# Optimization experiments

Hardware: AMD Instinct MI355X
Metric: run time of the kernel (lower is better)

Reference implementation:

```python
import jax, jax.numpy as jnp
import numpy as np

B, T, H, V, NT, NH, DFF = 2, 512, 768, 51865, 3, 4, 2048
EPS = 1e-5


def setup_inputs() -> dict:
    key = jax.random.key(0)
    ks = jax.random.split(key, 24)
    s = 0.02
    d = {
        "encoder_hidden": jax.random.normal(ks[0], (B, T, H), jnp.float32),
        "teacher_tokens": jax.random.randint(ks[1], (B, T, NT), 0, V, jnp.int32),
        "start_token": jax.random.normal(ks[2], (1, H), jnp.float32),
        "emb": jax.random.normal(ks[3], (V, H), jnp.float32) * s,
        # self-attention (torch MultiheadAttention packed qkv in_proj)
        "sa_in_w": jax.random.normal(ks[4], (3 * H, H), jnp.float32) * s,
        "sa_in_b": jnp.zeros((3 * H,), jnp.float32),
        "sa_out_w": jax.random.normal(ks[5], (H, H), jnp.float32) * s,
        "sa_out_b": jnp.zeros((H,), jnp.float32),
        # cross-attention
        "ca_in_w": jax.random.normal(ks[6], (3 * H, H), jnp.float32) * s,
        "ca_in_b": jnp.zeros((3 * H,), jnp.float32),
        "ca_out_w": jax.random.normal(ks[7], (H, H), jnp.float32) * s,
        "ca_out_b": jnp.zeros((H,), jnp.float32),
        # FFN
        "lin1_w": jax.random.normal(ks[8], (DFF, H), jnp.float32) * s,
        "lin1_b": jnp.zeros((DFF,), jnp.float32),
        "lin2_w": jax.random.normal(ks[9], (H, DFF), jnp.float32) * s,
        "lin2_b": jnp.zeros((H,), jnp.float32),
        # layer norms (post-norm TransformerDecoderLayer)
        "ln1_g": jnp.ones((H,), jnp.float32), "ln1_b": jnp.zeros((H,), jnp.float32),
        "ln2_g": jnp.ones((H,), jnp.float32), "ln2_b": jnp.zeros((H,), jnp.float32),
        "ln3_g": jnp.ones((H,), jnp.float32), "ln3_b": jnp.zeros((H,), jnp.float32),
        # output vocab projection (bias=False)
        "proj_w": jax.random.normal(ks[10], (V, H), jnp.float32) * s,
    }
    return d


def _ln(x, g, b):
    m = jnp.mean(x, -1, keepdims=True)
    v = jnp.mean(jnp.square(x - m), -1, keepdims=True)
    return (x - m) * jax.lax.rsqrt(v + EPS) * g + b


def _mha(xq, xkv, in_w, in_b, out_w, out_b, mask=None):
    # xq: (N, Lq, H), xkv: (N, Lk, H). torch packed in_proj: [Wq; Wk; Wv].
    h = xq.shape[-1]
    wq, wk, wv = jnp.split(in_w, 3, axis=0)
    bq, bk, bv = jnp.split(in_b, 3, axis=0)
    hd = h // NH
    q = (xq @ wq.T + bq).reshape(*xq.shape[:-1], NH, hd)
    k = (xkv @ wk.T + bk).reshape(*xkv.shape[:-1], NH, hd)
    v = (xkv @ wv.T + bv).reshape(*xkv.shape[:-1], NH, hd)
    scores = jnp.einsum("nqhd,nkhd->nhqk", q, k) / jnp.sqrt(jnp.float32(hd)).astype(q.dtype)
    if mask is not None:
        scores = scores + mask  # (Lq,Lk) additive causal mask
    a = jax.nn.softmax(scores, axis=-1)
    o = jnp.einsum("nhqk,nkhd->nqhd", a, v).reshape(*xq.shape[:-1], h)
    return o @ out_w.T + out_b


def _forward(encoder_hidden, teacher_tokens, start_token, emb,
             sa_in_w, sa_in_b, sa_out_w, sa_out_b,
             ca_in_w, ca_in_b, ca_out_w, ca_out_b,
             lin1_w, lin1_b, lin2_w, lin2_b,
             ln1_g, ln1_b, ln2_g, ln2_b, ln3_g, ln3_b, proj_w):
    b, t, h = encoder_hidden.shape
    nt = teacher_tokens.shape[-1]
    n = b * t
    # With teacher forcing + causal mask, step-i logits == position-i output of a
    # single decoder pass over [start, emb(teacher[..., :nt-1])] with memory of length 1.
    tok_emb = jnp.take(emb, teacher_tokens[:, :, : nt - 1], axis=0)  # (B,T,NT-1,H)
    start = jnp.broadcast_to(start_token.reshape(1, 1, 1, h), (b, t, 1, h))
    tgt = jnp.concatenate([start, tok_emb], axis=2).reshape(n, nt, h)  # (N,NT,H)
    mem = encoder_hidden.reshape(n, 1, h)  # (N,1,H)
    causal = jnp.where(jnp.triu(jnp.ones((nt, nt), bool), 1), -jnp.inf, 0.0).astype(tgt.dtype)
    # post-norm TransformerDecoderLayer (dropout=identity at eval)
    x = tgt
    x = _ln(x + _mha(x, x, sa_in_w, sa_in_b, sa_out_w, sa_out_b, causal), ln1_g, ln1_b)
    x = _ln(x + _mha(x, mem, ca_in_w, ca_in_b, ca_out_w, ca_out_b), ln2_g, ln2_b)
    ff = jax.nn.relu(x @ lin1_w.T + lin1_b) @ lin2_w.T + lin2_b
    x = _ln(x + ff, ln3_g, ln3_b)
    logits = x @ proj_w.T  # (N,NT,V)
    return logits.reshape(b, t, nt, -1)


def reference(encoder_hidden, teacher_tokens, start_token, emb,
              sa_in_w, sa_in_b, sa_out_w, sa_out_b,
              ca_in_w, ca_in_b, ca_out_w, ca_out_b,
              lin1_w, lin1_b, lin2_w, lin2_b,
              ln1_g, ln1_b, ln2_g, ln2_b, ln3_g, ln3_b, proj_w):
    return _forward(encoder_hidden, teacher_tokens, start_token, emb,
                    sa_in_w, sa_in_b, sa_out_w, sa_out_b,
                    ca_in_w, ca_in_b, ca_out_w, ca_out_b,
                    lin1_w, lin1_b, lin2_w, lin2_b,
                    ln1_g, ln1_b, ln2_g, ln2_b, ln3_g, ln3_b, proj_w)
```

## Files before the change

kernel.cpp:

```cpp
#include <hip/hip_runtime.h>

typedef __bf16 bf16;
typedef __bf16 bf16x4 __attribute__((ext_vector_type(4)));
typedef __bf16 bf16x8 __attribute__((ext_vector_type(8)));
typedef float f32x4 __attribute__((ext_vector_type(4)));

#define BM 128
#define BN 128
#define BK 32

__device__ __forceinline__ void async16(const void* g, void* l) {
    __builtin_amdgcn_global_load_lds(
        (__attribute__((address_space(1))) void*)g,
        (__attribute__((address_space(3))) void*)l,
        16, 0, 0);
}

__device__ __forceinline__ void stageA256(const bf16* A, int K, int brow, int r0,
                                          int k0, bf16* ldsA, int t, int wid) {
    int lr = t >> 3;
    int c  = (t & 7) ^ (lr & 7);
    const bf16* g = A + (size_t)(brow + r0 + lr) * K + k0 + c * 8;
    async16(g, ldsA + r0 * 64 + wid * 512);
}

__device__ __forceinline__ void stageB256(const bf16* W, int K, int bcol, int j,
                                          int k0, bf16* ldsB, int t, int wid) {
    int lr  = t >> 3;
    int R   = j * 64 + lr;
    int col = ((R >> 5) & 3) * 64 + (R >> 7) * 32 + (R & 31);
    int c   = (t & 7) ^ (lr & 7);
    const bf16* g = W + (size_t)(bcol + col) * K + k0 + c * 8;
    async16(g, ldsB + j * 4096 + wid * 512);
}

template<int VM, int QM, int QN>
__device__ __forceinline__ void mfma_phase256(const bf16* pa, const bf16* pb,
    int wm, int wn, int lane, f32x4 acc[8][4])
{
    const int l15 = lane & 15, l7 = lane & 7, lhi = lane >> 4;
    bf16x8 a[4][2], b[2][2];
    #pragma unroll
    for (int fi = 0; fi < 4; fi++)
        #pragma unroll
        for (int ks = 0; ks < 2; ks++)
            a[fi][ks] = *(const bf16x8*)(pa + (wm*128 + QM*64 + fi*16 + l15) * 64
                                            + ((ks*4 + lhi) ^ l7) * 8);
    #pragma unroll
    for (int fj = 0; fj < 2; fj++)
        #pragma unroll
        for (int ks = 0; ks < 2; ks++)
            b[fj][ks] = *(const bf16x8*)(pb + (QN*128 + wn*32 + fj*16 + l15) * 64
                                            + ((ks*4 + lhi) ^ l7) * 8);
    if (VM == 4)      asm volatile("s_waitcnt vmcnt(4)" ::: "memory");
    else if (VM == 2) asm volatile("s_waitcnt vmcnt(2)" ::: "memory");
    else              asm volatile("s_waitcnt vmcnt(0)" ::: "memory");
    __builtin_amdgcn_s_barrier();
    __builtin_amdgcn_s_setprio(1);
    #pragma unroll
    for (int fi = 0; fi < 4; fi++)
        #pragma unroll
        for (int fj = 0; fj < 2; fj++) {
            f32x4 c0 = acc[QM*4 + fi][QN*2 + fj];
            c0 = __builtin_amdgcn_mfma_f32_16x16x32_bf16(a[fi][0], b[fj][0], c0, 0,0,0);
            c0 = __builtin_amdgcn_mfma_f32_16x16x32_bf16(a[fi][1], b[fj][1], c0, 0,0,0);
            acc[QM*4 + fi][QN*2 + fj] = c0;
        }
    __builtin_amdgcn_s_setprio(0);
}

__global__ __launch_bounds__(512, 2) void gemm256(
    const bf16* __restrict__ A, const bf16* __restrict__ W,
    float* __restrict__ C, int K, int ldo, int Nstore, int nTilesM)
{
    __shared__ bf16 lds[2][2][16384];

    int nwg = gridDim.x;
    int orig = blockIdx.x;
    int q = nwg >> 3, r = nwg & 7, xcd = orig & 7, local = orig >> 3;
    int wgid = (xcd < r ? xcd * (q + 1) : r * (q + 1) + (xcd - r) * q) + local;
    const int brow = (wgid % nTilesM) * 256;
    const int bcol = (wgid / nTilesM) * 256;

    const int t = threadIdx.x;
    const int wid = t >> 6, lane = t & 63;
    const int wm = wid >> 2, wn = wid & 3;

    f32x4 acc[8][4] = {};
    const int nkt = K >> 6;

    {
        bf16* lA = &lds[0][0][0];
        bf16* lB = &lds[0][1][0];
        stageA256(A, K, brow,   0, 0, lA, t, wid);
        stageA256(A, K, brow, 128, 0, lA, t, wid);
        stageB256(W, K, bcol, 0, 0, lB, t, wid);
        stageB256(W, K, bcol, 1, 0, lB, t, wid);
        stageA256(A, K, brow,  64, 0, lA, t, wid);
        stageA256(A, K, brow, 192, 0, lA, t, wid);
        stageB256(W, K, bcol, 2, 0, lB, t, wid);
        stageB256(W, K, bcol, 3, 0, lB, t, wid);
        asm volatile("s_waitcnt vmcnt(4)" ::: "memory");
        __builtin_amdgcn_s_barrier();
    }

    for (int tt = 0; tt < nkt - 1; ++tt) {
        const int cur = tt & 1, nxt = cur ^ 1;
        const bf16* cA = &lds[cur][0][0];
        const bf16* cB = &lds[cur][1][0];
        bf16* nA = &lds[nxt][0][0];
        bf16* nB = &lds[nxt][1][0];
        const int k1 = (tt + 1) << 6;
        stageA256(A, K, brow,   0, k1, nA, t, wid);
        stageA256(A, K, brow, 128, k1, nA, t, wid);
        mfma_phase256<4, 0, 0>(cA, cB, wm, wn, lane, acc);
        stageB256(W, K, bcol, 0, k1, nB, t, wid);
        stageB256(W, K, bcol, 1, k1, nB, t, wid);
        mfma_phase256<4, 1, 0>(cA, cB, wm, wn, lane, acc);
        stageA256(A, K, brow,  64, k1, nA, t, wid);
        stageA256(A, K, brow, 192, k1, nA, t, wid);
        mfma_phase256<4, 0, 1>(cA, cB, wm, wn, lane, acc);
        stageB256(W, K, bcol, 2, k1, nB, t, wid);
        stageB256(W, K, bcol, 3, k1, nB, t, wid);
        mfma_phase256<4, 1, 1>(cA, cB, wm, wn, lane, acc);
    }
    {
        const int cur = (nkt - 1) & 1;
        const bf16* cA = &lds[cur][0][0];
        const bf16* cB = &lds[cur][1][0];
        mfma_phase256<2, 0, 0>(cA, cB, wm, wn, lane, acc);
        mfma_phase256<0, 1, 0>(cA, cB, wm, wn, lane, acc);
        mfma_phase256<0, 0, 1>(cA, cB, wm, wn, lane, acc);
        mfma_phase256<0, 1, 1>(cA, cB, wm, wn, lane, acc);
    }

    float* ldsf = (float*)&lds[0][0][0];
    const int l15 = lane & 15, lhi4 = (lane >> 4) * 4;
    #pragma unroll
    for (int h = 0; h < 2; h++) {
        __syncthreads();
        #pragma unroll
        for (int fi4 = 0; fi4 < 4; fi4++) {
            #pragma unroll
            for (int fj = 0; fj < 4; fj++) {
                f32x4 v = acc[h * 4 + fi4][fj];
                int row = wm * 64 + fi4 * 16 + lhi4;
                int col = wn * 64 + fj * 16 + l15;
                #pragma unroll
                for (int r2 = 0; r2 < 4; r2++)
                    ldsf[(row + r2) * 256 + col] = v[r2];
            }
        }
        __syncthreads();
        #pragma unroll
        for (int i = 0; i < 16; i++) {
            int c = i * 512 + t;
            int row = c >> 6, ch = c & 63;
            f32x4 v = *(const f32x4*)(ldsf + row * 256 + ch * 4);
            int grow = brow + (row >> 6) * 128 + h * 64 + (row & 63);
            int gcol = bcol + ch * 4;
            float* dst = C + (size_t)grow * ldo + gcol;
            if (gcol + 4 <= Nstore) {
                *(f32x4*)dst = v;
            } else {
                #pragma unroll
                for (int k2 = 0; k2 < 4; k2++)
                    if (gcol + k2 < Nstore) dst[k2] = v[k2];
            }
        }
    }
}

__global__ __launch_bounds__(256) void gemm_bt(
    const bf16* __restrict__ A, const bf16* __restrict__ W,
    const float* __restrict__ bias,
    float* __restrict__ outF, bf16* __restrict__ outB,
    int M, int K, int ldo, int Nstore, int relu)
{
    __shared__ bf16 As[BM * BK];
    __shared__ bf16 Ws[BN * BK];
    const int brow = blockIdx.y * BM;
    const int bcol = blockIdx.x * BN;
    const int t = threadIdx.x;
    const int wv = t >> 6;
    const int lane = t & 63;
    const int wrow = (wv >> 1) * 64;
    const int wcol = (wv & 1) * 64;

    f32x4 acc[4][4] = {};

    const int row0 = t >> 2;
    const int cg = (t & 3) * 8;
    const bf16* gA = A + (size_t)(brow + row0) * K + cg;
    const bf16* gW = W + (size_t)(bcol + row0) * K + cg;
    const size_t rstep = (size_t)64 * K;
    bf16* lA0 = As + wv * 512;
    bf16* lA1 = As + 2048 + wv * 512;
    bf16* lW0 = Ws + wv * 512;
    bf16* lW1 = Ws + 2048 + wv * 512;

    const int lrow = lane & 15;
    const int kg = (lane >> 4) * 8;

    for (int k0 = 0; k0 < K; k0 += BK) {
        if (k0) __syncthreads();
        async16(gA + k0, lA0);
        async16(gA + rstep + k0, lA1);
        async16(gW + k0, lW0);
        async16(gW + rstep + k0, lW1);
        __syncthreads();
        bf16x8 af[4], wf[4];
        #pragma unroll
        for (int i = 0; i < 4; i++)
            af[i] = *(const bf16x8*)(As + (wrow + i * 16 + lrow) * BK + kg);
        #pragma unroll
        for (int j = 0; j < 4; j++)
            wf[j] = *(const bf16x8*)(Ws + (wcol + j * 16 + lrow) * BK + kg);
        #pragma unroll
        for (int i = 0; i < 4; i++)
            #pragma unroll
            for (int j = 0; j < 4; j++)
                acc[i][j] = __builtin_amdgcn_mfma_f32_16x16x32_bf16(
                    af[i], wf[j], acc[i][j], 0, 0, 0);
    }

    const int lcol = lane & 15;
    const int rb = (lane >> 4) * 4;
    #pragma unroll
    for (int j = 0; j < 4; j++) {
        int n = bcol + wcol + j * 16 + lcol;
        if (n >= Nstore) continue;
        float bv = bias ? bias[n] : 0.f;
        #pragma unroll
        for (int i = 0; i < 4; i++) {
            #pragma unroll
            for (int r = 0; r < 4; r++) {
                int m = brow + wrow + i * 16 + rb + r;
                float v = acc[i][j][r] + bv;
                if (relu) v = fmaxf(v, 0.f);
                size_t off = (size_t)m * ldo + n;
                if (outF) outF[off] = v;
                if (outB) outB[off] = (bf16)v;
            }
        }
    }
}

__global__ __launch_bounds__(256) void cvt_bf16(
    const float* __restrict__ in, bf16* __restrict__ out,
    size_t nvalid, size_t ntotal)
{
    size_t i = ((size_t)blockIdx.x * 256 + threadIdx.x) * 4;
    if (i >= ntotal) return;
    bf16x4 r;
    if (i < nvalid) {
        f32x4 f = __builtin_nontemporal_load((const f32x4*)(in + i));
        r[0] = (bf16)f[0]; r[1] = (bf16)f[1]; r[2] = (bf16)f[2]; r[3] = (bf16)f[3];
    } else {
        r[0] = (bf16)0.f; r[1] = (bf16)0.f; r[2] = (bf16)0.f; r[3] = (bf16)0.f;
    }
    *(bf16x4*)(out + i) = r;
}

__global__ __launch_bounds__(256) void build_tgt(
    const float* __restrict__ start, const float* __restrict__ emb,
    const int* __restrict__ toks, float* __restrict__ outF, bf16* __restrict__ outB)
{
    int r = blockIdx.x;
    int n = r / 3, p = r % 3;
    const float* src = (p == 0) ? start : emb + (size_t)toks[n * 3 + (p - 1)] * 768;
    int t = threadIdx.x;
    #pragma unroll
    for (int j = 0; j < 3; j++) {
        int c = t + j * 256;
        float v = src[c];
        outF[(size_t)r * 768 + c] = v;
        outB[(size_t)r * 768 + c] = (bf16)v;
    }
}

__global__ __launch_bounds__(64) void attn3(
    const float* __restrict__ qkv, bf16* __restrict__ o)
{
    int blk = blockIdx.x;
    int n = blk >> 2, h = blk & 3;
    int lane = threadIdx.x;
    const float* base = qkv + (size_t)n * 3 * 2304 + h * 192;
    float q[3][3], k[3][3], v[3][3];
    #pragma unroll
    for (int p = 0; p < 3; p++)
        #pragma unroll
        for (int j = 0; j < 3; j++) {
            int d = lane + j * 64;
            q[p][j] = base[p * 2304 + d];
            k[p][j] = base[p * 2304 + 768 + d];
            v[p][j] = base[p * 2304 + 1536 + d];
        }
    float s[3][3];
    #pragma unroll
    for (int p = 0; p < 3; p++)
        #pragma unroll
        for (int pk = 0; pk < 3; pk++) {
            if (pk > p) continue;
            float ps = q[p][0] * k[pk][0] + q[p][1] * k[pk][1] + q[p][2] * k[pk][2];
            #pragma unroll
            for (int off = 32; off; off >>= 1) ps += __shfl_xor(ps, off);
            s[p][pk] = ps * 0.072168783648703220563f;
        }
    float a[3][3] = {};
    a[0][0] = 1.f;
    {
        float m = fmaxf(s[1][0], s[1][1]);
        float e0 = expf(s[1][0] - m), e1 = expf(s[1][1] - m);
        float inv = 1.f / (e0 + e1);
        a[1][0] = e0 * inv; a[1][1] = e1 * inv;
    }
    {
        float m = fmaxf(fmaxf(s[2][0], s[2][1]), s[2][2]);
        float e0 = expf(s[2][0] - m), e1 = expf(s[2][1] - m), e2 = expf(s[2][2] - m);
        float inv = 1.f / (e0 + e1 + e2);
        a[2][0] = e0 * inv; a[2][1] = e1 * inv; a[2][2] = e2 * inv;
    }
    bf16* ob = o + (size_t)n * 3 * 768 + h * 192;
    #pragma unroll
    for (int p = 0; p < 3; p++)
        #pragma unroll
        for (int j = 0; j < 3; j++) {
            float val = a[p][0] * v[0][j];
            if (p >= 1) val += a[p][1] * v[1][j];
            if (p >= 2) val += a[p][2] * v[2][j];
            ob[p * 768 + lane + j * 64] = (bf16)val;
        }
}

__global__ __launch_bounds__(256) void add_ln(
    const float* __restrict__ a, const float* __restrict__ b,
    const float* __restrict__ g, const float* __restrict__ be,
    float* __restrict__ outF, bf16* __restrict__ outB, int bcast)
{
    int r = blockIdx.x;
    int t = threadIdx.x;
    const float* ar = a + (size_t)r * 768;
    const float* br = b + (size_t)(bcast ? (r / 3) : r) * 768;
    float x[3];
    float s = 0.f, sq = 0.f;
    #pragma unroll
    for (int j = 0; j < 3; j++) {
        int c = t + j * 256;
        x[j] = ar[c] + br[c];
        s += x[j]; sq += x[j] * x[j];
    }
    #pragma unroll
    for (int off = 32; off; off >>= 1) {
        s += __shfl_xor(s, off);
        sq += __shfl_xor(sq, off);
    }
    __shared__ float ls[4], lq[4];
    int wv = t >> 6;
    if ((t & 63) == 0) { ls[wv] = s; lq[wv] = sq; }
    __syncthreads();
    s = ls[0] + ls[1] + ls[2] + ls[3];
    sq = lq[0] + lq[1] + lq[2] + lq[3];
    float mean = s * (1.f / 768.f);
    float var = sq * (1.f / 768.f) - mean * mean;
    float inv = rsqrtf(var + 1e-5f);
    #pragma unroll
    for (int j = 0; j < 3; j++) {
        int c = t + j * 256;
        float y = (x[j] - mean) * inv * g[c] + be[c];
        if (outF) outF[(size_t)r * 768 + c] = y;
        if (outB) outB[(size_t)r * 768 + c] = (bf16)y;
    }
}

static inline void run_gemm(const bf16* A, const bf16* W, const float* bias,
                            float* outF, bf16* outB, int M, int Npad, int K,
                            int ldo, int Nstore, int relu, hipStream_t s)
{
    dim3 grid(Npad / BN, M / BM);
    gemm_bt<<<grid, 256, 0, s>>>(A, W, bias, outF, outB, M, K, ldo, Nstore, relu);
}

static inline void run_cvt(const float* in, bf16* out, size_t nvalid,
                           size_t ntotal, hipStream_t s)
{
    int blocks = (int)((ntotal / 4 + 255) / 256);
    cvt_bf16<<<blocks, 256, 0, s>>>(in, out, nvalid, ntotal);
}

extern "C" void kernel_launch(void* const* d_in, const int* in_sizes, int n_in,
                              void* d_out, int out_size, void* d_ws, size_t ws_size,
                              hipStream_t stream)
{
    const float* enc      = (const float*)d_in[0];
    const int*   toks     = (const int*)d_in[1];
    const float* start    = (const float*)d_in[2];
    const float* emb      = (const float*)d_in[3];
    const float* sa_in_w  = (const float*)d_in[4];
    const float* sa_in_b  = (const float*)d_in[5];
    const float* sa_out_w = (const float*)d_in[6];
    const float* sa_out_b = (const float*)d_in[7];
    const float* ca_in_w  = (const float*)d_in[8];
    const float* ca_in_b  = (const float*)d_in[9];
    const float* ca_out_w = (const float*)d_in[10];
    const float* ca_out_b = (const float*)d_in[11];
    const float* lin1_w   = (const float*)d_in[12];
    const float* lin1_b   = (const float*)d_in[13];
    const float* lin2_w   = (const float*)d_in[14];
    const float* lin2_b   = (const float*)d_in[15];
    const float* ln1_g    = (const float*)d_in[16];
    const float* ln1_bb   = (const float*)d_in[17];
    const float* ln2_g    = (const float*)d_in[18];
    const float* ln2_bb   = (const float*)d_in[19];
    const float* ln3_g    = (const float*)d_in[20];
    const float* ln3_bb   = (const float*)d_in[21];
    const float* proj_w   = (const float*)d_in[22];
    float* out = (float*)d_out;

    const int NTOK = 3072;
    const int NM   = 1024;
    const int H    = 768;
    const int V    = 51865;
    const int VPAD = 51968;
    const int DFF  = 2048;

    char* p = (char*)d_ws;
    auto alloc = [&](size_t bytes) {
        void* r = (void*)p;
        p += (bytes + 255) & ~(size_t)255;
        return r;
    };
    float* tgt_f = (float*)alloc((size_t)NTOK * H * 4);
    float* x1_f  = (float*)alloc((size_t)NTOK * H * 4);
    float* x2_f  = (float*)alloc((size_t)NTOK * H * 4);
    float* big_f = (float*)alloc((size_t)NTOK * 2304 * 4);
    bf16*  actA  = (bf16*)alloc((size_t)NTOK * 2304 * 2);
    bf16*  actB  = (bf16*)alloc((size_t)NTOK * DFF * 2);
    bf16*  Wbf   = (bf16*)alloc((size_t)VPAD * H * 2);
    bf16*  mem_bf = actB;
    bf16*  v_bf   = actB + (size_t)NM * H;
    float* cao_f  = big_f + (size_t)NTOK * H;

    build_tgt<<<NTOK, 256, 0, stream>>>(start, emb, toks, tgt_f, actA);

    run_cvt(sa_in_w, Wbf, (size_t)2304 * H, (size_t)2304 * H, stream);
    run_gemm(actA, Wbf, sa_in_b, big_f, nullptr, NTOK, 2304, H, 2304, 2304, 0, stream);

    attn3<<<NM * 4, 64, 0, stream>>>(big_f, actA);

    run_cvt(sa_out_w, Wbf, (size_t)H * H, (size_t)H * H, stream);
    run_gemm(actA, Wbf, sa_out_b, big_f, nullptr, NTOK, H, H, H, H, 0, stream);

    add_ln<<<NTOK, 256, 0, stream>>>(tgt_f, big_f, ln1_g, ln1_bb, x1_f, nullptr, 0);

    run_cvt(enc, mem_bf, (size_t)NM * H, (size_t)NM * H, stream);
    run_cvt(ca_in_w + (size_t)1536 * H, Wbf, (size_t)H * H, (size_t)H * H, stream);
    run_gemm(mem_bf, Wbf, ca_in_b + 1536, nullptr, v_bf, NM, H, H, H, H, 0, stream);
    run_cvt(ca_out_w, Wbf, (size_t)H * H, (size_t)H * H, stream);
    run_gemm(v_bf, Wbf, ca_out_b, cao_f, nullptr, NM, H, H, H, H, 0, stream);

    add_ln<<<NTOK, 256, 0, stream>>>(x1_f, cao_f, ln2_g, ln2_bb, x2_f, actA, 1);

    run_cvt(lin1_w, Wbf, (size_t)DFF * H, (size_t)DFF * H, stream);
    run_gemm(actA, Wbf, lin1_b, nullptr, actB, NTOK, DFF, H, DFF, DFF, 1, stream);

    run_cvt(lin2_w, Wbf, (size_t)H * DFF, (size_t)H * DFF, stream);
    run_gemm(actB, Wbf, lin2_b, big_f, nullptr, NTOK, H, DFF, H, H, 0, stream);

    add_ln<<<NTOK, 256, 0, stream>>>(x2_f, big_f, ln3_g, ln3_bb, nullptr, actA, 0);

    run_cvt(proj_w, Wbf, (size_t)V * H, (size_t)VPAD * H, stream);
    {
        dim3 grid((NTOK / 256) * (VPAD / 256));
        gemm256<<<grid, 512, 0, stream>>>(actA, Wbf, out, H, V, V, NTOK / 256);
    }
}
```

Measured before the change: 623.1 us.

## Reload B fragments once per k-tile and halve barriers in the 256 GEMM

Restructures the gemm256 main loop from four phases per k-tile into two halves. B fragments for both column quadrants are read from LDS once and reused across both row halves, and there are two barriers per k-tile instead of four. The last tile is folded into the loop with a conditional vmcnt(0) wait. The epilogue's LDS staging of the fp32 tile gains an XOR swizzle to reduce bank conflicts. The trade-off is higher register pressure from holding all B fragments and less interleaving between global loads and MFMA work.

```diff
diff --git a/kernel.cpp b/kernel.cpp
--- a/kernel.cpp
+++ b/kernel.cpp
@@ -34,38 +34,46 @@
     async16(g, ldsB + j * 4096 + wid * 512);
 }
 
-template<int VM, int QM, int QN>
-__device__ __forceinline__ void mfma_phase256(const bf16* pa, const bf16* pb,
-    int wm, int wn, int lane, f32x4 acc[8][4])
-{
+__device__ __forceinline__ void ld_a256(const bf16* pa, int wm, int QM, int lane,
+                                        bf16x8 a[4][2]) {
     const int l15 = lane & 15, l7 = lane & 7, lhi = lane >> 4;
-    bf16x8 a[4][2], b[2][2];
     #pragma unroll
     for (int fi = 0; fi < 4; fi++)
         #pragma unroll
         for (int ks = 0; ks < 2; ks++)
             a[fi][ks] = *(const bf16x8*)(pa + (wm*128 + QM*64 + fi*16 + l15) * 64
                                             + ((ks*4 + lhi) ^ l7) * 8);
-    #pragma unroll
-    for (int fj = 0; fj < 2; fj++)
-        #pragma unroll
-        for (int ks = 0; ks < 2; ks++)
-            b[fj][ks] = *(const bf16x8*)(pb + (QN*128 + wn*32 + fj*16 + l15) * 64
-                                            + ((ks*4 + lhi) ^ l7) * 8);
-    if (VM == 4)      asm volatile("s_waitcnt vmcnt(4)" ::: "memory");
-    else if (VM == 2) asm volatile("s_waitcnt vmcnt(2)" ::: "memory");
-    else              asm volatile("s_waitcnt vmcnt(0)" ::: "memory");
-    __builtin_amdgcn_s_barrier();
+}
+
+__device__ __forceinline__ void ld_b256(const bf16* pb, int wn, int lane,
+                                        bf16x8 b[2][2][2]) {
+    const int l15 = lane & 15, l7 = lane & 7, lhi = lane >> 4;
+    #pragma unroll
+    for (int qn = 0; qn < 2; qn++)
+        #pragma unroll
+        for (int fj = 0; fj < 2; fj++)
+            #pragma unroll
+            for (int ks = 0; ks < 2; ks++)
+                b[qn][fj][ks] = *(const bf16x8*)(pb + (qn*128 + wn*32 + fj*16 + l15) * 64
+                                                    + ((ks*4 + lhi) ^ l7) * 8);
+}
+
+template<int QM>
+__device__ __forceinline__ void mfma_half(const bf16x8 a[4][2],
+                                          const bf16x8 b[2][2][2],
+                                          f32x4 acc[8][4]) {
     __builtin_amdgcn_s_setprio(1);
     #pragma unroll
     for (int fi = 0; fi < 4; fi++)
         #pragma unroll
-        for (int fj = 0; fj < 2; fj++) {
-            f32x4 c0 = acc[QM*4 + fi][QN*2 + fj];
-            c0 = __builtin_amdgcn_mfma_f32_16x16x32_bf16(a[fi][0], b[fj][0], c0, 0,0,0);
-            c0 = __builtin_amdgcn_mfma_f32_16x16x32_bf16(a[fi][1], b[fj][1], c0, 0,0,0);
-            acc[QM*4 + fi][QN*2 + fj] = c0;
-        }
+        for (int qn = 0; qn < 2; qn++)
+            #pragma unroll
+            for (int fj = 0; fj < 2; fj++) {
+                f32x4 c0 = acc[QM*4 + fi][qn*2 + fj];
+                c0 = __builtin_amdgcn_mfma_f32_16x16x32_bf16(a[fi][0], b[qn][fj][0], c0, 0,0,0);
+                c0 = __builtin_amdgcn_mfma_f32_16x16x32_bf16(a[fi][1], b[qn][fj][1], c0, 0,0,0);
+                acc[QM*4 + fi][qn*2 + fj] = c0;
+            }
     __builtin_amdgcn_s_setprio(0);
 }
 
@@ -100,38 +108,42 @@
         stageA256(A, K, brow, 192, 0, lA, t, wid);
         stageB256(W, K, bcol, 2, 0, lB, t, wid);
         stageB256(W, K, bcol, 3, 0, lB, t, wid);
-        asm volatile("s_waitcnt vmcnt(4)" ::: "memory");
-        __builtin_amdgcn_s_barrier();
-    }
-
-    for (int tt = 0; tt < nkt - 1; ++tt) {
-        const int cur = tt & 1, nxt = cur ^ 1;
+    }
+
+    bf16x8 b[2][2][2];
+    for (int tt = 0; tt < nkt; ++tt) {
+        const int cur = tt & 1;
         const bf16* cA = &lds[cur][0][0];
         const bf16* cB = &lds[cur][1][0];
-        bf16* nA = &lds[nxt][0][0];
-        bf16* nB = &lds[nxt][1][0];
+        bf16* nA = &lds[cur ^ 1][0][0];
+        bf16* nB = &lds[cur ^ 1][1][0];
         const int k1 = (tt + 1) << 6;
-        stageA256(A, K, brow,   0, k1, nA, t, wid);
-        stageA256(A, K, brow, 128, k1, nA, t, wid);
-        mfma_phase256<4, 0, 0>(cA, cB, wm, wn, lane, acc);
-        stageB256(W, K, bcol, 0, k1, nB, t, wid);
-        stageB256(W, K, bcol, 1, k1, nB, t, wid);
-        mfma_phase256<4, 1, 0>(cA, cB, wm, wn, lane, acc);
-        stageA256(A, K, brow,  64, k1, nA, t, wid);
-        stageA256(A, K, brow, 192, k1, nA, t, wid);
-        mfma_phase256<4, 0, 1>(cA, cB, wm, wn, lane, acc);
-        stageB256(W, K, bcol, 2, k1, nB, t, wid);
-        stageB256(W, K, bcol, 3, k1, nB, t, wid);
-        mfma_phase256<4, 1, 1>(cA, cB, wm, wn, lane, acc);
-    }
-    {
-        const int cur = (nkt - 1) & 1;
-        const bf16* cA = &lds[cur][0][0];
-        const bf16* cB = &lds[cur][1][0];
-        mfma_phase256<2, 0, 0>(cA, cB, wm, wn, lane, acc);
-        mfma_phase256<0, 1, 0>(cA, cB, wm, wn, lane, acc);
-        mfma_phase256<0, 0, 1>(cA, cB, wm, wn, lane, acc);
-        mfma_phase256<0, 1, 1>(cA, cB, wm, wn, lane, acc);
+        const bool last = (tt == nkt - 1);
+
+        if (!last) {
+            stageA256(A, K, brow,   0, k1, nA, t, wid);
+            stageA256(A, K, brow, 128, k1, nA, t, wid);
+            stageB256(W, K, bcol, 0, k1, nB, t, wid);
+            stageB256(W, K, bcol, 1, k1, nB, t, wid);
+            asm volatile("s_waitcnt vmcnt(4)" ::: "memory");
+        } else {
+            asm volatile("s_waitcnt vmcnt(0)" ::: "memory");
+        }
+        __builtin_amdgcn_s_barrier();
+        bf16x8 a[4][2];
+        ld_a256(cA, wm, 0, lane, a);
+        ld_b256(cB, wn, lane, b);
+        mfma_half<0>(a, b, acc);
+
+        if (!last) {
+            stageA256(A, K, brow,  64, k1, nA, t, wid);
+            stageA256(A, K, brow, 192, k1, nA, t, wid);
+            stageB256(W, K, bcol, 2, k1, nB, t, wid);
+            stageB256(W, K, bcol, 3, k1, nB, t, wid);
+        }
+        __builtin_amdgcn_s_barrier();
+        ld_a256(cA, wm, 1, lane, a);
+        mfma_half<1>(a, b, acc);
     }
 
     float* ldsf = (float*)&lds[0][0][0];
@@ -144,11 +156,13 @@
             #pragma unroll
             for (int fj = 0; fj < 4; fj++) {
                 f32x4 v = acc[h * 4 + fi4][fj];
-                int row = wm * 64 + fi4 * 16 + lhi4;
+                int row0 = wm * 64 + fi4 * 16 + lhi4;
                 int col = wn * 64 + fj * 16 + l15;
                 #pragma unroll
-                for (int r2 = 0; r2 < 4; r2++)
-                    ldsf[(row + r2) * 256 + col] = v[r2];
+                for (int r2 = 0; r2 < 4; r2++) {
+                    int row = row0 + r2;
+                    ldsf[row * 256 + (col ^ ((row & 12) << 1))] = v[r2];
+                }
             }
         }
         __syncthreads();
@@ -156,7 +170,8 @@
         for (int i = 0; i < 16; i++) {
             int c = i * 512 + t;
             int row = c >> 6, ch = c & 63;
-            f32x4 v = *(const f32x4*)(ldsf + row * 256 + ch * 4);
+            f32x4 v = *(const f32x4*)(ldsf + row * 256
+                                      + (ch ^ ((row & 12) >> 1)) * 4);
             int grow = brow + (row >> 6) * 128 + h * 64 + (row & 63);
             int gcol = bcol + ch * 4;
             float* dst = C + (size_t)grow * ldo + gcol;
```

Result: no change. 618.1 us (-0.8%).
